# Performance work log

Hardware: AMD Instinct MI355X
Metric: run time of the kernel (lower is better)

## Reference

```python
import jax, jax.numpy as jnp
import numpy as np

E = 8        # num_experts
H = 2048     # hidden_size
I = 1408     # intermediate_size
K = 2        # top_k
B, S = 1, 2048


def setup_inputs() -> dict:
    key = jax.random.key(0)
    k1, k2, k3, k4, k5 = jax.random.split(key, 5)
    hidden_states = jax.random.normal(k1, (B, S, H), dtype=jnp.float32)
    top_k_index = jax.random.randint(k2, (B, S, K), 0, E, dtype=jnp.int32)
    top_k_weights = jax.random.uniform(k3, (B, S, K), dtype=jnp.float32)
    # scaled init so activations stay O(1)
    gate_up_proj = jax.random.normal(k4, (E, 2 * I, H), dtype=jnp.float32) / np.sqrt(H)
    down_proj = jax.random.normal(k5, (E, H, I), dtype=jnp.float32) / np.sqrt(I)
    return {
        "hidden_states": hidden_states,
        "top_k_index": top_k_index,
        "top_k_weights": top_k_weights,
        "gate_up_proj": gate_up_proj,
        "down_proj": down_proj,
    }


def reference(hidden_states, top_k_index, top_k_weights, gate_up_proj, down_proj):
    orig_shape = hidden_states.shape
    x = hidden_states.reshape(-1, H)            # [T, H]
    idx = top_k_index.reshape(-1, K)            # [T, K] int32
    w = top_k_weights.reshape(-1, K)            # [T, K]
    out = jnp.zeros_like(x)
    for e in range(E):
        # combine weight for tokens routed to expert e (0 if not routed)
        we = jnp.sum(w * (idx == e).astype(w.dtype), axis=-1)   # [T]
        gu = x @ gate_up_proj[e].T                              # [T, 2I]
        gate, up = gu[:, :I], gu[:, I:]
        h = jax.nn.silu(gate) * up                              # [T, I]
        y = h @ down_proj[e].T                                  # [T, H]
        out = out + we[:, None] * y
    return out.reshape(orig_shape)
```

## Files before the change

kernel.cpp:

```cpp
#include <hip/hip_runtime.h>
#include <hip/hip_bf16.h>

#define E_ 8
#define H_ 2048
#define I_ 1408
#define S_ 2048
#define NPAIR 4096
#define MAXMT 32

#define KT1 64
#define KT2 44

#define WGBLK 22528
#define WDBLK 11264
#define XBLK   2048

typedef short bf16x8 __attribute__((ext_vector_type(8)));
typedef ushort u16x8 __attribute__((ext_vector_type(8)));
typedef float f32x4  __attribute__((ext_vector_type(4)));

__device__ inline bf16x8 pack8(float4 a, float4 b) {
    bf16x8 r;
    const float v[8] = {a.x, a.y, a.z, a.w, b.x, b.y, b.z, b.w};
#pragma unroll
    for (int j = 0; j < 8; ++j) {
        __hip_bfloat16 t = __float2bfloat16(v[j]);
        r[j] = *reinterpret_cast<short*>(&t);
    }
    return r;
}

__device__ __forceinline__ void gload16(const ushort* g, ushort* l) {
    __builtin_amdgcn_global_load_lds(
        (const __attribute__((address_space(1))) void*)g,
        (__attribute__((address_space(3))) void*)l,
        16, 0, 0);
}

__global__ __launch_bounds__(256)
void convert_all(const float* __restrict__ wg, const float* __restrict__ wd,
                 const float* __restrict__ x, const int* __restrict__ tki,
                 ushort* __restrict__ wgb, ushort* __restrict__ wdb,
                 ushort* __restrict__ xb,
                 int* __restrict__ counts, int* __restrict__ bases,
                 int* __restrict__ tok, int* __restrict__ inv) {
    const int b = blockIdx.x;
    const int tid = threadIdx.x;
    if (b < WGBLK + WDBLK + XBLK) {
        const float* src;
        ushort* dst;
        size_t off;
        if (b < WGBLK)              { src = wg; dst = wgb; off = (size_t)b * 2048; }
        else if (b < WGBLK + WDBLK) { src = wd; dst = wdb; off = (size_t)(b - WGBLK) * 2048; }
        else                        { src = x;  dst = xb;  off = (size_t)(b - WGBLK - WDBLK) * 2048; }
        const size_t i = off + (size_t)tid * 8;
        const float4 a = *(const float4*)(src + i);
        const float4 c = *(const float4*)(src + i + 4);
        *(bf16x8*)(dst + i) = pack8(a, c);
        return;
    }
    __shared__ int cnt[E_];
    __shared__ int cur[E_];
    if (tid < E_) cnt[tid] = 0;
    __syncthreads();
    for (int p = tid; p < NPAIR; p += 256)
        atomicAdd(&cnt[tki[p]], 1);
    __syncthreads();
    if (tid == 0) {
        int bb = 0;
        for (int e = 0; e < E_; ++e) {
            counts[e] = cnt[e];
            bases[e]  = bb;
            cur[e]    = bb;
            bb += cnt[e];
        }
    }
    __syncthreads();
    for (int p = tid; p < NPAIR; p += 256) {
        const int e = tki[p];
        const int pos = atomicAdd(&cur[e], 1);
        tok[pos] = p >> 1;
        inv[p]   = pos;
    }
}

__global__ __launch_bounds__(256, 2)
void moe_gemm1(const ushort* __restrict__ xb,
               const ushort* __restrict__ wgb,
               const int* __restrict__ counts,
               const int* __restrict__ bases,
               const int* __restrict__ tok,
               ushort* __restrict__ hbuf) {
    const int e  = blockIdx.y & (E_ - 1);
    const int mt = blockIdx.y >> 3;
    const int count = counts[e];
    if (mt * 128 >= count) return;
    const int base = bases[e];
    const int nt = blockIdx.x;
    const int n0 = nt * 128;
    const ushort* wgbe = wgb + (size_t)e * (2 * I_) * H_;

    __shared__ alignas(16) ushort sm[24576];

    const int tid  = threadIdx.x;
    const int lane = tid & 63;
    const int wid  = tid >> 6;
    const int wm = wid & 1, wn = wid >> 1;
    const int lr = lane & 15, lq = lane >> 4;

    const f32x4 vzero = {0.f, 0.f, 0.f, 0.f};
    f32x4 accg[4][4], accu[4][4];
#pragma unroll
    for (int mi = 0; mi < 4; ++mi)
#pragma unroll
        for (int ni = 0; ni < 4; ++ni) { accg[mi][ni] = vzero; accu[mi][ni] = vzero; }

    const int srow = tid >> 2;
    const int sc8  = (tid & 3) * 8;
    const int ia0 = mt * 128 + srow, ia1 = ia0 + 64;
    const ushort* ap0 = xb + (size_t)(ia0 < count ? tok[base + ia0] : 0) * H_ + sc8;
    const ushort* ap1 = xb + (size_t)(ia1 < count ? tok[base + ia1] : 0) * H_ + sc8;
    const ushort* gp0 = wgbe + (size_t)(n0 + srow) * H_ + sc8;
    const ushort* gp1 = gp0 + (size_t)64 * H_;
    const ushort* up0 = wgbe + (size_t)(I_ + n0 + srow) * H_ + sc8;
    const ushort* up1 = up0 + (size_t)64 * H_;

    const int d0 = tid * 8, d1 = tid * 8 + 2048;

    {
        ushort* bA = sm; ushort* bG = sm + 4096; ushort* bU = sm + 8192;
        gload16(ap0, bA + d0); gload16(ap1, bA + d1);
        gload16(gp0, bG + d0); gload16(gp1, bG + d1);
        gload16(up0, bU + d0); gload16(up1, bU + d1);
    }

    for (int kt = 0; kt < KT1; ++kt) {
        ushort* curb = sm + (kt & 1) * 12288;
        if (kt + 1 < KT1) {
            ap0 += 32; ap1 += 32; gp0 += 32; gp1 += 32; up0 += 32; up1 += 32;
            ushort* nb = sm + ((kt + 1) & 1) * 12288;
            gload16(ap0, nb + d0);        gload16(ap1, nb + d1);
            gload16(gp0, nb + 4096 + d0); gload16(gp1, nb + 4096 + d1);
            gload16(up0, nb + 8192 + d0); gload16(up1, nb + 8192 + d1);
            asm volatile("s_waitcnt vmcnt(6)" ::: "memory");
        } else {
            asm volatile("s_waitcnt vmcnt(0)" ::: "memory");
        }
        __builtin_amdgcn_s_barrier();
        __builtin_amdgcn_sched_barrier(0);

        const ushort* As = curb;
        const ushort* Bg = curb + 4096;
        const ushort* Bu = curb + 8192;
        bf16x8 a[4], bg[4], bu[4];
#pragma unroll
        for (int mi = 0; mi < 4; ++mi)
            a[mi] = *(const bf16x8*)&As[(wm * 64 + mi * 16 + lr) * 32 + lq * 8];
#pragma unroll
        for (int ni = 0; ni < 4; ++ni) {
            bg[ni] = *(const bf16x8*)&Bg[(wn * 64 + ni * 16 + lr) * 32 + lq * 8];
            bu[ni] = *(const bf16x8*)&Bu[(wn * 64 + ni * 16 + lr) * 32 + lq * 8];
        }
#pragma unroll
        for (int mi = 0; mi < 4; ++mi)
#pragma unroll
            for (int ni = 0; ni < 4; ++ni) {
                accg[mi][ni] = __builtin_amdgcn_mfma_f32_16x16x32_bf16(a[mi], bg[ni], accg[mi][ni], 0, 0, 0);
                accu[mi][ni] = __builtin_amdgcn_mfma_f32_16x16x32_bf16(a[mi], bu[ni], accu[mi][ni], 0, 0, 0);
            }
        __builtin_amdgcn_sched_barrier(0);
        __builtin_amdgcn_s_barrier();
    }

    ushort* Ht = sm;
#pragma unroll
    for (int mi = 0; mi < 4; ++mi)
#pragma unroll
        for (int r = 0; r < 4; ++r) {
            const int row = wm * 64 + mi * 16 + lq * 4 + r;
#pragma unroll
            for (int ni = 0; ni < 4; ++ni) {
                const int col = wn * 64 + ni * 16 + lr;
                const float g = accg[mi][ni][r];
                const float u = accu[mi][ni][r];
                const float h = (g / (1.0f + __expf(-g))) * u;
                __hip_bfloat16 hb = __float2bfloat16(h);
                Ht[row * 136 + col] = *reinterpret_cast<ushort*>(&hb);
            }
        }
    __syncthreads();
#pragma unroll
    for (int p = 0; p < 8; ++p) {
        const int slot = p * 256 + tid;
        const int row = slot >> 4;
        const int cc  = (slot & 15) * 8;
        const int gi = mt * 128 + row;
        if (gi < count)
            *(uint4*)&hbuf[(size_t)(base + gi) * I_ + n0 + cc] = *(const uint4*)&Ht[row * 136 + cc];
    }
}

__global__ __launch_bounds__(256, 2)
void moe_gemm2(const ushort* __restrict__ hbuf,
               const ushort* __restrict__ wdb,
               const int* __restrict__ counts,
               const int* __restrict__ bases,
               ushort* __restrict__ ybuf) {
    const int e  = blockIdx.y & (E_ - 1);
    const int mt = blockIdx.y >> 3;
    const int count = counts[e];
    if (mt * 128 >= count) return;
    const int base = bases[e];
    const int nt = blockIdx.x;
    const int n0 = nt * 128;
    const ushort* wdbe = wdb + (size_t)e * H_ * I_;

    __shared__ alignas(16) ushort sm[17408];

    const int tid  = threadIdx.x;
    const int lane = tid & 63;
    const int wid  = tid >> 6;
    const int wm = wid & 1, wn = wid >> 1;
    const int lr = lane & 15, lq = lane >> 4;

    const f32x4 vzero = {0.f, 0.f, 0.f, 0.f};
    f32x4 acc[4][4];
#pragma unroll
    for (int mi = 0; mi < 4; ++mi)
#pragma unroll
        for (int ni = 0; ni < 4; ++ni) acc[mi][ni] = vzero;

    const int srow = tid >> 2;
    const int sc8  = (tid & 3) * 8;
    const int ia0 = mt * 128 + srow, ia1 = ia0 + 64;
    const ushort* ap0 = hbuf + (size_t)(base + (ia0 < count ? ia0 : 0)) * I_ + sc8;
    const ushort* ap1 = hbuf + (size_t)(base + (ia1 < count ? ia1 : 0)) * I_ + sc8;
    const ushort* bp0 = wdbe + (size_t)(n0 + srow) * I_ + sc8;
    const ushort* bp1 = bp0 + (size_t)64 * I_;

    const int d0 = tid * 8, d1 = tid * 8 + 2048;

    {
        ushort* bA = sm; ushort* bB = sm + 4096;
        gload16(ap0, bA + d0); gload16(ap1, bA + d1);
        gload16(bp0, bB + d0); gload16(bp1, bB + d1);
    }

    for (int kt = 0; kt < KT2; ++kt) {
        ushort* curb = sm + (kt & 1) * 8192;
        if (kt + 1 < KT2) {
            ap0 += 32; ap1 += 32; bp0 += 32; bp1 += 32;
            ushort* nb = sm + ((kt + 1) & 1) * 8192;
            gload16(ap0, nb + d0);        gload16(ap1, nb + d1);
            gload16(bp0, nb + 4096 + d0); gload16(bp1, nb + 4096 + d1);
            asm volatile("s_waitcnt vmcnt(4)" ::: "memory");
        } else {
            asm volatile("s_waitcnt vmcnt(0)" ::: "memory");
        }
        __builtin_amdgcn_s_barrier();
        __builtin_amdgcn_sched_barrier(0);

        const ushort* As = curb;
        const ushort* Bs = curb + 4096;
        bf16x8 a[4], b[4];
#pragma unroll
        for (int mi = 0; mi < 4; ++mi)
            a[mi] = *(const bf16x8*)&As[(wm * 64 + mi * 16 + lr) * 32 + lq * 8];
#pragma unroll
        for (int ni = 0; ni < 4; ++ni)
            b[ni] = *(const bf16x8*)&Bs[(wn * 64 + ni * 16 + lr) * 32 + lq * 8];
#pragma unroll
        for (int mi = 0; mi < 4; ++mi)
#pragma unroll
            for (int ni = 0; ni < 4; ++ni)
                acc[mi][ni] = __builtin_amdgcn_mfma_f32_16x16x32_bf16(a[mi], b[ni], acc[mi][ni], 0, 0, 0);
        __builtin_amdgcn_sched_barrier(0);
        __builtin_amdgcn_s_barrier();
    }

    ushort* Yt = sm;
#pragma unroll
    for (int mi = 0; mi < 4; ++mi)
#pragma unroll
        for (int r = 0; r < 4; ++r) {
            const int row = wm * 64 + mi * 16 + lq * 4 + r;
#pragma unroll
            for (int ni = 0; ni < 4; ++ni) {
                const int col = wn * 64 + ni * 16 + lr;
                __hip_bfloat16 yb = __float2bfloat16(acc[mi][ni][r]);
                Yt[row * 136 + col] = *reinterpret_cast<ushort*>(&yb);
            }
        }
    __syncthreads();
#pragma unroll
    for (int p = 0; p < 8; ++p) {
        const int slot = p * 256 + tid;
        const int row = slot >> 4;
        const int cc  = (slot & 15) * 8;
        const int gi = mt * 128 + row;
        if (gi < count)
            *(uint4*)&ybuf[(size_t)(base + gi) * H_ + n0 + cc] = *(const uint4*)&Yt[row * 136 + cc];
    }
}

__global__ void moe_combine(const ushort* __restrict__ ybuf,
                            const int* __restrict__ inv,
                            const float* __restrict__ tkw,
                            float* __restrict__ out) {
    const int t = blockIdx.x;
    const int c8 = threadIdx.x * 8;
    const int p0 = inv[2 * t], p1 = inv[2 * t + 1];
    const float w0 = tkw[2 * t], w1 = tkw[2 * t + 1];
    const u16x8 y0 = *(const u16x8*)(ybuf + (size_t)p0 * H_ + c8);
    const u16x8 y1 = *(const u16x8*)(ybuf + (size_t)p1 * H_ + c8);
    float o[8];
#pragma unroll
    for (int j = 0; j < 8; ++j) {
        const unsigned f0 = ((unsigned)y0[j]) << 16;
        const unsigned f1 = ((unsigned)y1[j]) << 16;
        o[j] = w0 * __uint_as_float(f0) + w1 * __uint_as_float(f1);
    }
    float* dst = out + (size_t)t * H_ + c8;
    *(float4*)dst       = make_float4(o[0], o[1], o[2], o[3]);
    *(float4*)(dst + 4) = make_float4(o[4], o[5], o[6], o[7]);
}

extern "C" void kernel_launch(void* const* d_in, const int* in_sizes, int n_in,
                              void* d_out, int out_size, void* d_ws, size_t ws_size,
                              hipStream_t stream) {
    const float* x   = (const float*)d_in[0];
    const int*   tki = (const int*)d_in[1];
    const float* tkw = (const float*)d_in[2];
    const float* wg  = (const float*)d_in[3];
    const float* wd  = (const float*)d_in[4];
    float* out = (float*)d_out;

    char* p = (char*)d_ws;
    int* counts = (int*)p;  p += 32;
    int* bases  = (int*)p;  p += 32;
    int* tok    = (int*)p;  p += NPAIR * sizeof(int);
    int* inv    = (int*)p;  p += NPAIR * sizeof(int);
    ushort* xb   = (ushort*)p; p += (size_t)S_ * H_ * 2;
    ushort* hbuf = (ushort*)p; p += (size_t)NPAIR * I_ * 2;
    ushort* ybuf = (ushort*)p; p += (size_t)NPAIR * H_ * 2;
    ushort* wgb  = (ushort*)p; p += (size_t)E_ * (2 * I_) * H_ * 2;
    ushort* wdb  = (ushort*)p; p += (size_t)E_ * H_ * I_ * 2;

    convert_all<<<dim3(WGBLK + WDBLK + XBLK + 1), 256, 0, stream>>>(
        wg, wd, x, tki, wgb, wdb, xb, counts, bases, tok, inv);
    moe_gemm1<<<dim3(I_ / 128, E_ * MAXMT), 256, 0, stream>>>(xb, wgb, counts, bases, tok, hbuf);
    moe_gemm2<<<dim3(H_ / 128, E_ * MAXMT), 256, 0, stream>>>(hbuf, wdb, counts, bases, ybuf);
    moe_combine<<<dim3(S_), 256, 0, stream>>>(ybuf, inv, tkw, out);
}
```

Measured before the change: 474.0 us.

## Use grid-stride conversion and loop over M tiles inside the MoE GEMM blocks

The fp32-to-bf16 conversion kernel now runs with a fixed 2048 blocks that grid-stride over the weight and activation chunks, instead of one block per chunk. Both grouped GEMM kernels launch only 4 M-slots per expert and loop over M tiles with stride 4. This replaces the old grid of 32 slots per expert, where most blocks exited early. The aim is to cut launch and empty-block overhead. The risk is that experts with more than 512 routed pairs now process their extra tile serially in the same block, which lengthens the tail of the GEMMs.

```diff
diff --git a/kernel.cpp b/kernel.cpp
--- a/kernel.cpp
+++ b/kernel.cpp
@@ -6,7 +6,6 @@
 #define I_ 1408
 #define S_ 2048
 #define NPAIR 4096
-#define MAXMT 32
 
 #define KT1 64
 #define KT2 44
@@ -14,6 +13,7 @@
 #define WGBLK 22528
 #define WDBLK 11264
 #define XBLK   2048
+#define CVT_BLOCKS 2048
 
 typedef short bf16x8 __attribute__((ext_vector_type(8)));
 typedef ushort u16x8 __attribute__((ext_vector_type(8)));
@@ -46,17 +46,26 @@
                  int* __restrict__ tok, int* __restrict__ inv) {
     const int b = blockIdx.x;
     const int tid = threadIdx.x;
-    if (b < WGBLK + WDBLK + XBLK) {
-        const float* src;
-        ushort* dst;
-        size_t off;
-        if (b < WGBLK)              { src = wg; dst = wgb; off = (size_t)b * 2048; }
-        else if (b < WGBLK + WDBLK) { src = wd; dst = wdb; off = (size_t)(b - WGBLK) * 2048; }
-        else                        { src = x;  dst = xb;  off = (size_t)(b - WGBLK - WDBLK) * 2048; }
-        const size_t i = off + (size_t)tid * 8;
-        const float4 a = *(const float4*)(src + i);
-        const float4 c = *(const float4*)(src + i + 4);
-        *(bf16x8*)(dst + i) = pack8(a, c);
+    if (b < CVT_BLOCKS) {
+        const int t8 = tid * 8;
+        for (int c = b; c < WGBLK; c += CVT_BLOCKS) {
+            const size_t i = (size_t)c * 2048 + t8;
+            const float4 a = *(const float4*)(wg + i);
+            const float4 d = *(const float4*)(wg + i + 4);
+            *(bf16x8*)(wgb + i) = pack8(a, d);
+        }
+        for (int c = b; c < WDBLK; c += CVT_BLOCKS) {
+            const size_t i = (size_t)c * 2048 + t8;
+            const float4 a = *(const float4*)(wd + i);
+            const float4 d = *(const float4*)(wd + i + 4);
+            *(bf16x8*)(wdb + i) = pack8(a, d);
+        }
+        for (int c = b; c < XBLK; c += CVT_BLOCKS) {
+            const size_t i = (size_t)c * 2048 + t8;
+            const float4 a = *(const float4*)(x + i);
+            const float4 d = *(const float4*)(x + i + 4);
+            *(bf16x8*)(xb + i) = pack8(a, d);
+        }
         return;
     }
     __shared__ int cnt[E_];
@@ -92,9 +101,8 @@
                const int* __restrict__ tok,
                ushort* __restrict__ hbuf) {
     const int e  = blockIdx.y & (E_ - 1);
-    const int mt = blockIdx.y >> 3;
+    const int m0 = blockIdx.y >> 3;
     const int count = counts[e];
-    if (mt * 128 >= count) return;
     const int base = bases[e];
     const int nt = blockIdx.x;
     const int n0 = nt * 128;
@@ -108,95 +116,98 @@
     const int wm = wid & 1, wn = wid >> 1;
     const int lr = lane & 15, lq = lane >> 4;
 
-    const f32x4 vzero = {0.f, 0.f, 0.f, 0.f};
-    f32x4 accg[4][4], accu[4][4];
-#pragma unroll
-    for (int mi = 0; mi < 4; ++mi)
-#pragma unroll
-        for (int ni = 0; ni < 4; ++ni) { accg[mi][ni] = vzero; accu[mi][ni] = vzero; }
-
     const int srow = tid >> 2;
     const int sc8  = (tid & 3) * 8;
-    const int ia0 = mt * 128 + srow, ia1 = ia0 + 64;
-    const ushort* ap0 = xb + (size_t)(ia0 < count ? tok[base + ia0] : 0) * H_ + sc8;
-    const ushort* ap1 = xb + (size_t)(ia1 < count ? tok[base + ia1] : 0) * H_ + sc8;
-    const ushort* gp0 = wgbe + (size_t)(n0 + srow) * H_ + sc8;
-    const ushort* gp1 = gp0 + (size_t)64 * H_;
-    const ushort* up0 = wgbe + (size_t)(I_ + n0 + srow) * H_ + sc8;
-    const ushort* up1 = up0 + (size_t)64 * H_;
-
     const int d0 = tid * 8, d1 = tid * 8 + 2048;
-
-    {
-        ushort* bA = sm; ushort* bG = sm + 4096; ushort* bU = sm + 8192;
-        gload16(ap0, bA + d0); gload16(ap1, bA + d1);
-        gload16(gp0, bG + d0); gload16(gp1, bG + d1);
-        gload16(up0, bU + d0); gload16(up1, bU + d1);
-    }
-
-    for (int kt = 0; kt < KT1; ++kt) {
-        ushort* curb = sm + (kt & 1) * 12288;
-        if (kt + 1 < KT1) {
-            ap0 += 32; ap1 += 32; gp0 += 32; gp1 += 32; up0 += 32; up1 += 32;
-            ushort* nb = sm + ((kt + 1) & 1) * 12288;
-            gload16(ap0, nb + d0);        gload16(ap1, nb + d1);
-            gload16(gp0, nb + 4096 + d0); gload16(gp1, nb + 4096 + d1);
-            gload16(up0, nb + 8192 + d0); gload16(up1, nb + 8192 + d1);
-            asm volatile("s_waitcnt vmcnt(6)" ::: "memory");
-        } else {
-            asm volatile("s_waitcnt vmcnt(0)" ::: "memory");
-        }
-        __builtin_amdgcn_s_barrier();
-        __builtin_amdgcn_sched_barrier(0);
-
-        const ushort* As = curb;
-        const ushort* Bg = curb + 4096;
-        const ushort* Bu = curb + 8192;
-        bf16x8 a[4], bg[4], bu[4];
+    const f32x4 vzero = {0.f, 0.f, 0.f, 0.f};
+
+    for (int mt = m0; mt * 128 < count; mt += 4) {
+        f32x4 accg[4][4], accu[4][4];
 #pragma unroll
         for (int mi = 0; mi < 4; ++mi)
-            a[mi] = *(const bf16x8*)&As[(wm * 64 + mi * 16 + lr) * 32 + lq * 8];
-#pragma unroll
-        for (int ni = 0; ni < 4; ++ni) {
-            bg[ni] = *(const bf16x8*)&Bg[(wn * 64 + ni * 16 + lr) * 32 + lq * 8];
-            bu[ni] = *(const bf16x8*)&Bu[(wn * 64 + ni * 16 + lr) * 32 + lq * 8];
-        }
+#pragma unroll
+            for (int ni = 0; ni < 4; ++ni) { accg[mi][ni] = vzero; accu[mi][ni] = vzero; }
+
+        const int ia0 = mt * 128 + srow, ia1 = ia0 + 64;
+        const ushort* ap0 = xb + (size_t)(ia0 < count ? tok[base + ia0] : 0) * H_ + sc8;
+        const ushort* ap1 = xb + (size_t)(ia1 < count ? tok[base + ia1] : 0) * H_ + sc8;
+        const ushort* gp0 = wgbe + (size_t)(n0 + srow) * H_ + sc8;
+        const ushort* gp1 = gp0 + (size_t)64 * H_;
+        const ushort* up0 = wgbe + (size_t)(I_ + n0 + srow) * H_ + sc8;
+        const ushort* up1 = up0 + (size_t)64 * H_;
+
+        {
+            ushort* bA = sm; ushort* bG = sm + 4096; ushort* bU = sm + 8192;
+            gload16(ap0, bA + d0); gload16(ap1, bA + d1);
+            gload16(gp0, bG + d0); gload16(gp1, bG + d1);
+            gload16(up0, bU + d0); gload16(up1, bU + d1);
+        }
+
+        for (int kt = 0; kt < KT1; ++kt) {
+            ushort* curb = sm + (kt & 1) * 12288;
+            if (kt + 1 < KT1) {
+                ap0 += 32; ap1 += 32; gp0 += 32; gp1 += 32; up0 += 32; up1 += 32;
+                ushort* nb = sm + ((kt + 1) & 1) * 12288;
+                gload16(ap0, nb + d0);        gload16(ap1, nb + d1);
+                gload16(gp0, nb + 4096 + d0); gload16(gp1, nb + 4096 + d1);
+                gload16(up0, nb + 8192 + d0); gload16(up1, nb + 8192 + d1);
+                asm volatile("s_waitcnt vmcnt(6)" ::: "memory");
+            } else {
+                asm volatile("s_waitcnt vmcnt(0)" ::: "memory");
+            }
+            __builtin_amdgcn_s_barrier();
+            __builtin_amdgcn_sched_barrier(0);
+
+            const ushort* As = curb;
+            const ushort* Bg = curb + 4096;
+            const ushort* Bu = curb + 8192;
+            bf16x8 a[4], bg[4], bu[4];
+#pragma unroll
+            for (int mi = 0; mi < 4; ++mi)
+                a[mi] = *(const bf16x8*)&As[(wm * 64 + mi * 16 + lr) * 32 + lq * 8];
+#pragma unroll
+            for (int ni = 0; ni < 4; ++ni) {
+                bg[ni] = *(const bf16x8*)&Bg[(wn * 64 + ni * 16 + lr) * 32 + lq * 8];
+                bu[ni] = *(const bf16x8*)&Bu[(wn * 64 + ni * 16 + lr) * 32 + lq * 8];
+            }
+#pragma unroll
+            for (int mi = 0; mi < 4; ++mi)
+#pragma unroll
+                for (int ni = 0; ni < 4; ++ni) {
+                    accg[mi][ni] = __builtin_amdgcn_mfma_f32_16x16x32_bf16(a[mi], bg[ni], accg[mi][ni], 0, 0, 0);
+                    accu[mi][ni] = __builtin_amdgcn_mfma_f32_16x16x32_bf16(a[mi], bu[ni], accu[mi][ni], 0, 0, 0);
+                }
+            __builtin_amdgcn_sched_barrier(0);
+            __builtin_amdgcn_s_barrier();
+        }
+
+        ushort* Ht = sm;
 #pragma unroll
         for (int mi = 0; mi < 4; ++mi)
 #pragma unroll
-            for (int ni = 0; ni < 4; ++ni) {
-                accg[mi][ni] = __builtin_amdgcn_mfma_f32_16x16x32_bf16(a[mi], bg[ni], accg[mi][ni], 0, 0, 0);
-                accu[mi][ni] = __builtin_amdgcn_mfma_f32_16x16x32_bf16(a[mi], bu[ni], accu[mi][ni], 0, 0, 0);
-            }
-        __builtin_amdgcn_sched_barrier(0);
-        __builtin_amdgcn_s_barrier();
-    }
-
-    ushort* Ht = sm;
-#pragma unroll
-    for (int mi = 0; mi < 4; ++mi)
-#pragma unroll
-        for (int r = 0; r < 4; ++r) {
-            const int row = wm * 64 + mi * 16 + lq * 4 + r;
-#pragma unroll
-            for (int ni = 0; ni < 4; ++ni) {
-                const int col = wn * 64 + ni * 16 + lr;
-                const float g = accg[mi][ni][r];
-                const float u = accu[mi][ni][r];
-                const float h = (g / (1.0f + __expf(-g))) * u;
-                __hip_bfloat16 hb = __float2bfloat16(h);
-                Ht[row * 136 + col] = *reinterpret_cast<ushort*>(&hb);
-            }
-        }
-    __syncthreads();
-#pragma unroll
-    for (int p = 0; p < 8; ++p) {
-        const int slot = p * 256 + tid;
-        const int row = slot >> 4;
-        const int cc  = (slot & 15) * 8;
-        const int gi = mt * 128 + row;
-        if (gi < count)
-            *(uint4*)&hbuf[(size_t)(base + gi) * I_ + n0 + cc] = *(const uint4*)&Ht[row * 136 + cc];
+            for (int r = 0; r < 4; ++r) {
+                const int row = wm * 64 + mi * 16 + lq * 4 + r;
+#pragma unroll
+                for (int ni = 0; ni < 4; ++ni) {
+                    const int col = wn * 64 + ni * 16 + lr;
+                    const float g = accg[mi][ni][r];
+                    const float u = accu[mi][ni][r];
+                    const float h = (g / (1.0f + __expf(-g))) * u;
+                    __hip_bfloat16 hb = __float2bfloat16(h);
+                    Ht[row * 136 + col] = *reinterpret_cast<ushort*>(&hb);
+                }
+            }
+        __syncthreads();
+#pragma unroll
+        for (int p = 0; p < 8; ++p) {
+            const int slot = p * 256 + tid;
+            const int row = slot >> 4;
+            const int cc  = (slot & 15) * 8;
+            const int gi = mt * 128 + row;
+            if (gi < count)
+                *(uint4*)&hbuf[(size_t)(base + gi) * I_ + n0 + cc] = *(const uint4*)&Ht[row * 136 + cc];
+        }
+        __syncthreads();
     }
 }
 
@@ -207,9 +218,8 @@
                const int* __restrict__ bases,
                ushort* __restrict__ ybuf) {
     const int e  = blockIdx.y & (E_ - 1);
-    const int mt = blockIdx.y >> 3;
+    const int m0 = blockIdx.y >> 3;
     const int count = counts[e];
-    if (mt * 128 >= count) return;
     const int base = bases[e];
     const int nt = blockIdx.x;
     const int n0 = nt * 128;
@@ -223,83 +233,86 @@
     const int wm = wid & 1, wn = wid >> 1;
     const int lr = lane & 15, lq = lane >> 4;
 
-    const f32x4 vzero = {0.f, 0.f, 0.f, 0.f};
-    f32x4 acc[4][4];
-#pragma unroll
-    for (int mi = 0; mi < 4; ++mi)
-#pragma unroll
-        for (int ni = 0; ni < 4; ++ni) acc[mi][ni] = vzero;
-
     const int srow = tid >> 2;
     const int sc8  = (tid & 3) * 8;
-    const int ia0 = mt * 128 + srow, ia1 = ia0 + 64;
-    const ushort* ap0 = hbuf + (size_t)(base + (ia0 < count ? ia0 : 0)) * I_ + sc8;
-    const ushort* ap1 = hbuf + (size_t)(base + (ia1 < count ? ia1 : 0)) * I_ + sc8;
-    const ushort* bp0 = wdbe + (size_t)(n0 + srow) * I_ + sc8;
-    const ushort* bp1 = bp0 + (size_t)64 * I_;
-
     const int d0 = tid * 8, d1 = tid * 8 + 2048;
-
-    {
-        ushort* bA = sm; ushort* bB = sm + 4096;
-        gload16(ap0, bA + d0); gload16(ap1, bA + d1);
-        gload16(bp0, bB + d0); gload16(bp1, bB + d1);
-    }
-
-    for (int kt = 0; kt < KT2; ++kt) {
-        ushort* curb = sm + (kt & 1) * 8192;
-        if (kt + 1 < KT2) {
-            ap0 += 32; ap1 += 32; bp0 += 32; bp1 += 32;
-            ushort* nb = sm + ((kt + 1) & 1) * 8192;
-            gload16(ap0, nb + d0);        gload16(ap1, nb + d1);
-            gload16(bp0, nb + 4096 + d0); gload16(bp1, nb + 4096 + d1);
-            asm volatile("s_waitcnt vmcnt(4)" ::: "memory");
-        } else {
-            asm volatile("s_waitcnt vmcnt(0)" ::: "memory");
-        }
-        __builtin_amdgcn_s_barrier();
-        __builtin_amdgcn_sched_barrier(0);
-
-        const ushort* As = curb;
-        const ushort* Bs = curb + 4096;
-        bf16x8 a[4], b[4];
+    const f32x4 vzero = {0.f, 0.f, 0.f, 0.f};
+
+    for (int mt = m0; mt * 128 < count; mt += 4) {
+        f32x4 acc[4][4];
 #pragma unroll
         for (int mi = 0; mi < 4; ++mi)
-            a[mi] = *(const bf16x8*)&As[(wm * 64 + mi * 16 + lr) * 32 + lq * 8];
-#pragma unroll
-        for (int ni = 0; ni < 4; ++ni)
-            b[ni] = *(const bf16x8*)&Bs[(wn * 64 + ni * 16 + lr) * 32 + lq * 8];
+#pragma unroll
+            for (int ni = 0; ni < 4; ++ni) acc[mi][ni] = vzero;
+
+        const int ia0 = mt * 128 + srow, ia1 = ia0 + 64;
+        const ushort* ap0 = hbuf + (size_t)(base + (ia0 < count ? ia0 : 0)) * I_ + sc8;
+        const ushort* ap1 = hbuf + (size_t)(base + (ia1 < count ? ia1 : 0)) * I_ + sc8;
+        const ushort* bp0 = wdbe + (size_t)(n0 + srow) * I_ + sc8;
+        const ushort* bp1 = bp0 + (size_t)64 * I_;
+
+        {
+            ushort* bA = sm; ushort* bB = sm + 4096;
+            gload16(ap0, bA + d0); gload16(ap1, bA + d1);
+            gload16(bp0, bB + d0); gload16(bp1, bB + d1);
+        }
+
+        for (int kt = 0; kt < KT2; ++kt) {
+            ushort* curb = sm + (kt & 1) * 8192;
+            if (kt + 1 < KT2) {
+                ap0 += 32; ap1 += 32; bp0 += 32; bp1 += 32;
+                ushort* nb = sm + ((kt + 1) & 1) * 8192;
+                gload16(ap0, nb + d0);        gload16(ap1, nb + d1);
+                gload16(bp0, nb + 4096 + d0); gload16(bp1, nb + 4096 + d1);
+                asm volatile("s_waitcnt vmcnt(4)" ::: "memory");
+            } else {
+                asm volatile("s_waitcnt vmcnt(0)" ::: "memory");
+            }
+            __builtin_amdgcn_s_barrier();
+            __builtin_amdgcn_sched_barrier(0);
+
+            const ushort* As = curb;
+            const ushort* Bs = curb + 4096;
+            bf16x8 a[4], b[4];
+#pragma unroll
+            for (int mi = 0; mi < 4; ++mi)
+                a[mi] = *(const bf16x8*)&As[(wm * 64 + mi * 16 + lr) * 32 + lq * 8];
+#pragma unroll
+            for (int ni = 0; ni < 4; ++ni)
+                b[ni] = *(const bf16x8*)&Bs[(wn * 64 + ni * 16 + lr) * 32 + lq * 8];
+#pragma unroll
+            for (int mi = 0; mi < 4; ++mi)
+#pragma unroll
+                for (int ni = 0; ni < 4; ++ni)
+                    acc[mi][ni] = __builtin_amdgcn_mfma_f32_16x16x32_bf16(a[mi], b[ni], acc[mi][ni], 0, 0, 0);
+            __builtin_amdgcn_sched_barrier(0);
+            __builtin_amdgcn_s_barrier();
+        }
+
+        ushort* Yt = sm;
 #pragma unroll
         for (int mi = 0; mi < 4; ++mi)
 #pragma unroll
-            for (int ni = 0; ni < 4; ++ni)
-                acc[mi][ni] = __builtin_amdgcn_mfma_f32_16x16x32_bf16(a[mi], b[ni], acc[mi][ni], 0, 0, 0);
-        __builtin_amdgcn_sched_barrier(0);
-        __builtin_amdgcn_s_barrier();
-    }
-
-    ushort* Yt = sm;
-#pragma unroll
-    for (int mi = 0; mi < 4; ++mi)
-#pragma unroll
-        for (int r = 0; r < 4; ++r) {
-            const int row = wm * 64 + mi * 16 + lq * 4 + r;
-#pragma unroll
-            for (int ni = 0; ni < 4; ++ni) {
-                const int col = wn * 64 + ni * 16 + lr;
-                __hip_bfloat16 yb = __float2bfloat16(acc[mi][ni][r]);
-                Yt[row * 136 + col] = *reinterpret_cast<ushort*>(&yb);
-            }
-        }
-    __syncthreads();
-#pragma unroll
-    for (int p = 0; p < 8; ++p) {
-        const int slot = p * 256 + tid;
-        const int row = slot >> 4;
-        const int cc  = (slot & 15) * 8;
-        const int gi = mt * 128 + row;
-        if (gi < count)
-            *(uint4*)&ybuf[(size_t)(base + gi) * H_ + n0 + cc] = *(const uint4*)&Yt[row * 136 + cc];
+            for (int r = 0; r < 4; ++r) {
+                const int row = wm * 64 + mi * 16 + lq * 4 + r;
+#pragma unroll
+                for (int ni = 0; ni < 4; ++ni) {
+                    const int col = wn * 64 + ni * 16 + lr;
+                    __hip_bfloat16 yb = __float2bfloat16(acc[mi][ni][r]);
+                    Yt[row * 136 + col] = *reinterpret_cast<ushort*>(&yb);
+                }
+            }
+        __syncthreads();
+#pragma unroll
+        for (int p = 0; p < 8; ++p) {
+            const int slot = p * 256 + tid;
+            const int row = slot >> 4;
+            const int cc  = (slot & 15) * 8;
+            const int gi = mt * 128 + row;
+            if (gi < count)
+                *(uint4*)&ybuf[(size_t)(base + gi) * H_ + n0 + cc] = *(const uint4*)&Yt[row * 136 + cc];
+        }
+        __syncthreads();
     }
 }
 
@@ -346,9 +359,9 @@
     ushort* wgb  = (ushort*)p; p += (size_t)E_ * (2 * I_) * H_ * 2;
     ushort* wdb  = (ushort*)p; p += (size_t)E_ * H_ * I_ * 2;
 
-    convert_all<<<dim3(WGBLK + WDBLK + XBLK + 1), 256, 0, stream>>>(
+    convert_all<<<dim3(CVT_BLOCKS + 1), 256, 0, stream>>>(
         wg, wd, x, tki, wgb, wdb, xb, counts, bases, tok, inv);
-    moe_gemm1<<<dim3(I_ / 128, E_ * MAXMT), 256, 0, stream>>>(xb, wgb, counts, bases, tok, hbuf);
-    moe_gemm2<<<dim3(H_ / 128, E_ * MAXMT), 256, 0, stream>>>(hbuf, wdb, counts, bases, ybuf);
+    moe_gemm1<<<dim3(I_ / 128, E_ * 4), 256, 0, stream>>>(xb, wgb, counts, bases, tok, hbuf);
+    moe_gemm2<<<dim3(H_ / 128, E_ * 4), 256, 0, stream>>>(hbuf, wdb, counts, bases, ybuf);
     moe_combine<<<dim3(S_), 256, 0, stream>>>(ybuf, inv, tkw, out);
 }
```

Measured after the change: 508.2 us. 7.2% more time.

## Fuse down-proj weight conversion into gemm1 and use persistent M-tile loops

Applied to the files above, without the earlier changes.

The fp32-to-bf16 conversion of the down-projection weights moves out of the standalone convert kernel and into the start of every gemm1 block, with each of the 704 blocks converting 16 chunks. The aim is to overlap that conversion traffic with gemm1 compute and shrink the convert pass. Both GEMMs also drop the fixed 32-M-tile grid (mostly early-exit blocks) for 8 blocks per expert that loop over M tiles with stride 8, which cuts idle block launches. In exchange, long-tailed experts are serialized within fewer blocks, and the conversion adds memory traffic at the head of gemm1.

```diff
diff --git a/kernel.cpp b/kernel.cpp
--- a/kernel.cpp
+++ b/kernel.cpp
@@ -6,14 +6,14 @@
 #define I_ 1408
 #define S_ 2048
 #define NPAIR 4096
-#define MAXMT 32
 
 #define KT1 64
 #define KT2 44
 
 #define WGBLK 22528
+#define XBLK   2048
 #define WDBLK 11264
-#define XBLK   2048
+#define WD_PER_BLK 16
 
 typedef short bf16x8 __attribute__((ext_vector_type(8)));
 typedef ushort u16x8 __attribute__((ext_vector_type(8)));
@@ -38,21 +38,19 @@
 }
 
 __global__ __launch_bounds__(256)
-void convert_all(const float* __restrict__ wg, const float* __restrict__ wd,
-                 const float* __restrict__ x, const int* __restrict__ tki,
-                 ushort* __restrict__ wgb, ushort* __restrict__ wdb,
-                 ushort* __restrict__ xb,
+void convert_all(const float* __restrict__ wg, const float* __restrict__ x,
+                 const int* __restrict__ tki,
+                 ushort* __restrict__ wgb, ushort* __restrict__ xb,
                  int* __restrict__ counts, int* __restrict__ bases,
                  int* __restrict__ tok, int* __restrict__ inv) {
     const int b = blockIdx.x;
     const int tid = threadIdx.x;
-    if (b < WGBLK + WDBLK + XBLK) {
+    if (b < WGBLK + XBLK) {
         const float* src;
         ushort* dst;
         size_t off;
-        if (b < WGBLK)              { src = wg; dst = wgb; off = (size_t)b * 2048; }
-        else if (b < WGBLK + WDBLK) { src = wd; dst = wdb; off = (size_t)(b - WGBLK) * 2048; }
-        else                        { src = x;  dst = xb;  off = (size_t)(b - WGBLK - WDBLK) * 2048; }
+        if (b < WGBLK) { src = wg; dst = wgb; off = (size_t)b * 2048; }
+        else           { src = x;  dst = xb;  off = (size_t)(b - WGBLK) * 2048; }
         const size_t i = off + (size_t)tid * 8;
         const float4 a = *(const float4*)(src + i);
         const float4 c = *(const float4*)(src + i + 4);
@@ -87,14 +85,29 @@
 __global__ __launch_bounds__(256, 2)
 void moe_gemm1(const ushort* __restrict__ xb,
                const ushort* __restrict__ wgb,
+               const float* __restrict__ wd,
+               ushort* __restrict__ wdb,
                const int* __restrict__ counts,
                const int* __restrict__ bases,
                const int* __restrict__ tok,
                ushort* __restrict__ hbuf) {
+    const int tid  = threadIdx.x;
+
+    {
+        const int bid = blockIdx.y * gridDim.x + blockIdx.x;
+        const size_t t8 = (size_t)tid * 8;
+#pragma unroll
+        for (int j = 0; j < WD_PER_BLK; ++j) {
+            const size_t i = ((size_t)(bid * WD_PER_BLK + j)) * 2048 + t8;
+            const float4 a = *(const float4*)(wd + i);
+            const float4 c = *(const float4*)(wd + i + 4);
+            *(bf16x8*)(wdb + i) = pack8(a, c);
+        }
+    }
+
     const int e  = blockIdx.y & (E_ - 1);
-    const int mt = blockIdx.y >> 3;
+    const int m0 = blockIdx.y >> 3;
     const int count = counts[e];
-    if (mt * 128 >= count) return;
     const int base = bases[e];
     const int nt = blockIdx.x;
     const int n0 = nt * 128;
@@ -102,101 +115,103 @@
 
     __shared__ alignas(16) ushort sm[24576];
 
-    const int tid  = threadIdx.x;
     const int lane = tid & 63;
     const int wid  = tid >> 6;
     const int wm = wid & 1, wn = wid >> 1;
     const int lr = lane & 15, lq = lane >> 4;
 
-    const f32x4 vzero = {0.f, 0.f, 0.f, 0.f};
-    f32x4 accg[4][4], accu[4][4];
-#pragma unroll
-    for (int mi = 0; mi < 4; ++mi)
-#pragma unroll
-        for (int ni = 0; ni < 4; ++ni) { accg[mi][ni] = vzero; accu[mi][ni] = vzero; }
-
     const int srow = tid >> 2;
     const int sc8  = (tid & 3) * 8;
-    const int ia0 = mt * 128 + srow, ia1 = ia0 + 64;
-    const ushort* ap0 = xb + (size_t)(ia0 < count ? tok[base + ia0] : 0) * H_ + sc8;
-    const ushort* ap1 = xb + (size_t)(ia1 < count ? tok[base + ia1] : 0) * H_ + sc8;
-    const ushort* gp0 = wgbe + (size_t)(n0 + srow) * H_ + sc8;
-    const ushort* gp1 = gp0 + (size_t)64 * H_;
-    const ushort* up0 = wgbe + (size_t)(I_ + n0 + srow) * H_ + sc8;
-    const ushort* up1 = up0 + (size_t)64 * H_;
-
     const int d0 = tid * 8, d1 = tid * 8 + 2048;
-
-    {
-        ushort* bA = sm; ushort* bG = sm + 4096; ushort* bU = sm + 8192;
-        gload16(ap0, bA + d0); gload16(ap1, bA + d1);
-        gload16(gp0, bG + d0); gload16(gp1, bG + d1);
-        gload16(up0, bU + d0); gload16(up1, bU + d1);
-    }
-
-    for (int kt = 0; kt < KT1; ++kt) {
-        ushort* curb = sm + (kt & 1) * 12288;
-        if (kt + 1 < KT1) {
-            ap0 += 32; ap1 += 32; gp0 += 32; gp1 += 32; up0 += 32; up1 += 32;
-            ushort* nb = sm + ((kt + 1) & 1) * 12288;
-            gload16(ap0, nb + d0);        gload16(ap1, nb + d1);
-            gload16(gp0, nb + 4096 + d0); gload16(gp1, nb + 4096 + d1);
-            gload16(up0, nb + 8192 + d0); gload16(up1, nb + 8192 + d1);
-            asm volatile("s_waitcnt vmcnt(6)" ::: "memory");
-        } else {
-            asm volatile("s_waitcnt vmcnt(0)" ::: "memory");
-        }
-        __builtin_amdgcn_s_barrier();
-        __builtin_amdgcn_sched_barrier(0);
-
-        const ushort* As = curb;
-        const ushort* Bg = curb + 4096;
-        const ushort* Bu = curb + 8192;
-        bf16x8 a[4], bg[4], bu[4];
+    const f32x4 vzero = {0.f, 0.f, 0.f, 0.f};
+
+    for (int mt = m0; mt * 128 < count; mt += 8) {
+        f32x4 accg[4][4], accu[4][4];
 #pragma unroll
         for (int mi = 0; mi < 4; ++mi)
-            a[mi] = *(const bf16x8*)&As[(wm * 64 + mi * 16 + lr) * 32 + lq * 8];
-#pragma unroll
-        for (int ni = 0; ni < 4; ++ni) {
-            bg[ni] = *(const bf16x8*)&Bg[(wn * 64 + ni * 16 + lr) * 32 + lq * 8];
-            bu[ni] = *(const bf16x8*)&Bu[(wn * 64 + ni * 16 + lr) * 32 + lq * 8];
-        }
+#pragma unroll
+            for (int ni = 0; ni < 4; ++ni) { accg[mi][ni] = vzero; accu[mi][ni] = vzero; }
+
+        const int ia0 = mt * 128 + srow, ia1 = ia0 + 64;
+        const ushort* ap0 = xb + (size_t)(ia0 < count ? tok[base + ia0] : 0) * H_ + sc8;
+        const ushort* ap1 = xb + (size_t)(ia1 < count ? tok[base + ia1] : 0) * H_ + sc8;
+        const ushort* gp0 = wgbe + (size_t)(n0 + srow) * H_ + sc8;
+        const ushort* gp1 = gp0 + (size_t)64 * H_;
+        const ushort* up0 = wgbe + (size_t)(I_ + n0 + srow) * H_ + sc8;
+        const ushort* up1 = up0 + (size_t)64 * H_;
+
+        {
+            ushort* bA = sm; ushort* bG = sm + 4096; ushort* bU = sm + 8192;
+            gload16(ap0, bA + d0); gload16(ap1, bA + d1);
+            gload16(gp0, bG + d0); gload16(gp1, bG + d1);
+            gload16(up0, bU + d0); gload16(up1, bU + d1);
+        }
+
+        for (int kt = 0; kt < KT1; ++kt) {
+            ushort* curb = sm + (kt & 1) * 12288;
+            if (kt + 1 < KT1) {
+                ap0 += 32; ap1 += 32; gp0 += 32; gp1 += 32; up0 += 32; up1 += 32;
+                ushort* nb = sm + ((kt + 1) & 1) * 12288;
+                gload16(ap0, nb + d0);        gload16(ap1, nb + d1);
+                gload16(gp0, nb + 4096 + d0); gload16(gp1, nb + 4096 + d1);
+                gload16(up0, nb + 8192 + d0); gload16(up1, nb + 8192 + d1);
+                asm volatile("s_waitcnt vmcnt(6)" ::: "memory");
+            } else {
+                asm volatile("s_waitcnt vmcnt(0)" ::: "memory");
+            }
+            __builtin_amdgcn_s_barrier();
+            __builtin_amdgcn_sched_barrier(0);
+
+            const ushort* As = curb;
+            const ushort* Bg = curb + 4096;
+            const ushort* Bu = curb + 8192;
+            bf16x8 a[4], bg[4], bu[4];
+#pragma unroll
+            for (int mi = 0; mi < 4; ++mi)
+                a[mi] = *(const bf16x8*)&As[(wm * 64 + mi * 16 + lr) * 32 + lq * 8];
+#pragma unroll
+            for (int ni = 0; ni < 4; ++ni) {
+                bg[ni] = *(const bf16x8*)&Bg[(wn * 64 + ni * 16 + lr) * 32 + lq * 8];
+                bu[ni] = *(const bf16x8*)&Bu[(wn * 64 + ni * 16 + lr) * 32 + lq * 8];
+            }
+#pragma unroll
+            for (int mi = 0; mi < 4; ++mi)
+#pragma unroll
+                for (int ni = 0; ni < 4; ++ni) {
+                    accg[mi][ni] = __builtin_amdgcn_mfma_f32_16x16x32_bf16(a[mi], bg[ni], accg[mi][ni], 0, 0, 0);
+                    accu[mi][ni] = __builtin_amdgcn_mfma_f32_16x16x32_bf16(a[mi], bu[ni], accu[mi][ni], 0, 0, 0);
+                }
+            __builtin_amdgcn_sched_barrier(0);
+            __builtin_amdgcn_s_barrier();
+        }
+
+        ushort* Ht = sm;
 #pragma unroll
         for (int mi = 0; mi < 4; ++mi)
 #pragma unroll
-            for (int ni = 0; ni < 4; ++ni) {
-                accg[mi][ni] = __builtin_amdgcn_mfma_f32_16x16x32_bf16(a[mi], bg[ni], accg[mi][ni], 0, 0, 0);
-                accu[mi][ni] = __builtin_amdgcn_mfma_f32_16x16x32_bf16(a[mi], bu[ni], accu[mi][ni], 0, 0, 0);
-            }
-        __builtin_amdgcn_sched_barrier(0);
-        __builtin_amdgcn_s_barrier();
-    }
-
-    ushort* Ht = sm;
-#pragma unroll
-    for (int mi = 0; mi < 4; ++mi)
-#pragma unroll
-        for (int r = 0; r < 4; ++r) {
-            const int row = wm * 64 + mi * 16 + lq * 4 + r;
-#pragma unroll
-            for (int ni = 0; ni < 4; ++ni) {
-                const int col = wn * 64 + ni * 16 + lr;
-                const float g = accg[mi][ni][r];
-                const float u = accu[mi][ni][r];
-                const float h = (g / (1.0f + __expf(-g))) * u;
-                __hip_bfloat16 hb = __float2bfloat16(h);
-                Ht[row * 136 + col] = *reinterpret_cast<ushort*>(&hb);
-            }
-        }
-    __syncthreads();
-#pragma unroll
-    for (int p = 0; p < 8; ++p) {
-        const int slot = p * 256 + tid;
-        const int row = slot >> 4;
-        const int cc  = (slot & 15) * 8;
-        const int gi = mt * 128 + row;
-        if (gi < count)
-            *(uint4*)&hbuf[(size_t)(base + gi) * I_ + n0 + cc] = *(const uint4*)&Ht[row * 136 + cc];
+            for (int r = 0; r < 4; ++r) {
+                const int row = wm * 64 + mi * 16 + lq * 4 + r;
+#pragma unroll
+                for (int ni = 0; ni < 4; ++ni) {
+                    const int col = wn * 64 + ni * 16 + lr;
+                    const float g = accg[mi][ni][r];
+                    const float u = accu[mi][ni][r];
+                    const float h = (g / (1.0f + __expf(-g))) * u;
+                    __hip_bfloat16 hb = __float2bfloat16(h);
+                    Ht[row * 136 + col] = *reinterpret_cast<ushort*>(&hb);
+                }
+            }
+        __syncthreads();
+#pragma unroll
+        for (int p = 0; p < 8; ++p) {
+            const int slot = p * 256 + tid;
+            const int row = slot >> 4;
+            const int cc  = (slot & 15) * 8;
+            const int gi = mt * 128 + row;
+            if (gi < count)
+                *(uint4*)&hbuf[(size_t)(base + gi) * I_ + n0 + cc] = *(const uint4*)&Ht[row * 136 + cc];
+        }
+        __syncthreads();
     }
 }
 
@@ -207,9 +222,8 @@
                const int* __restrict__ bases,
                ushort* __restrict__ ybuf) {
     const int e  = blockIdx.y & (E_ - 1);
-    const int mt = blockIdx.y >> 3;
+    const int m0 = blockIdx.y >> 3;
     const int count = counts[e];
-    if (mt * 128 >= count) return;
     const int base = bases[e];
     const int nt = blockIdx.x;
     const int n0 = nt * 128;
@@ -223,83 +237,86 @@
     const int wm = wid & 1, wn = wid >> 1;
     const int lr = lane & 15, lq = lane >> 4;
 
-    const f32x4 vzero = {0.f, 0.f, 0.f, 0.f};
-    f32x4 acc[4][4];
-#pragma unroll
-    for (int mi = 0; mi < 4; ++mi)
-#pragma unroll
-        for (int ni = 0; ni < 4; ++ni) acc[mi][ni] = vzero;
-
     const int srow = tid >> 2;
     const int sc8  = (tid & 3) * 8;
-    const int ia0 = mt * 128 + srow, ia1 = ia0 + 64;
-    const ushort* ap0 = hbuf + (size_t)(base + (ia0 < count ? ia0 : 0)) * I_ + sc8;
-    const ushort* ap1 = hbuf + (size_t)(base + (ia1 < count ? ia1 : 0)) * I_ + sc8;
-    const ushort* bp0 = wdbe + (size_t)(n0 + srow) * I_ + sc8;
-    const ushort* bp1 = bp0 + (size_t)64 * I_;
-
     const int d0 = tid * 8, d1 = tid * 8 + 2048;
-
-    {
-        ushort* bA = sm; ushort* bB = sm + 4096;
-        gload16(ap0, bA + d0); gload16(ap1, bA + d1);
-        gload16(bp0, bB + d0); gload16(bp1, bB + d1);
-    }
-
-    for (int kt = 0; kt < KT2; ++kt) {
-        ushort* curb = sm + (kt & 1) * 8192;
-        if (kt + 1 < KT2) {
-            ap0 += 32; ap1 += 32; bp0 += 32; bp1 += 32;
-            ushort* nb = sm + ((kt + 1) & 1) * 8192;
-            gload16(ap0, nb + d0);        gload16(ap1, nb + d1);
-            gload16(bp0, nb + 4096 + d0); gload16(bp1, nb + 4096 + d1);
-            asm volatile("s_waitcnt vmcnt(4)" ::: "memory");
-        } else {
-            asm volatile("s_waitcnt vmcnt(0)" ::: "memory");
-        }
-        __builtin_amdgcn_s_barrier();
-        __builtin_amdgcn_sched_barrier(0);
-
-        const ushort* As = curb;
-        const ushort* Bs = curb + 4096;
-        bf16x8 a[4], b[4];
+    const f32x4 vzero = {0.f, 0.f, 0.f, 0.f};
+
+    for (int mt = m0; mt * 128 < count; mt += 8) {
+        f32x4 acc[4][4];
 #pragma unroll
         for (int mi = 0; mi < 4; ++mi)
-            a[mi] = *(const bf16x8*)&As[(wm * 64 + mi * 16 + lr) * 32 + lq * 8];
-#pragma unroll
-        for (int ni = 0; ni < 4; ++ni)
-            b[ni] = *(const bf16x8*)&Bs[(wn * 64 + ni * 16 + lr) * 32 + lq * 8];
+#pragma unroll
+            for (int ni = 0; ni < 4; ++ni) acc[mi][ni] = vzero;
+
+        const int ia0 = mt * 128 + srow, ia1 = ia0 + 64;
+        const ushort* ap0 = hbuf + (size_t)(base + (ia0 < count ? ia0 : 0)) * I_ + sc8;
+        const ushort* ap1 = hbuf + (size_t)(base + (ia1 < count ? ia1 : 0)) * I_ + sc8;
+        const ushort* bp0 = wdbe + (size_t)(n0 + srow) * I_ + sc8;
+        const ushort* bp1 = bp0 + (size_t)64 * I_;
+
+        {
+            ushort* bA = sm; ushort* bB = sm + 4096;
+            gload16(ap0, bA + d0); gload16(ap1, bA + d1);
+            gload16(bp0, bB + d0); gload16(bp1, bB + d1);
+        }
+
+        for (int kt = 0; kt < KT2; ++kt) {
+            ushort* curb = sm + (kt & 1) * 8192;
+            if (kt + 1 < KT2) {
+                ap0 += 32; ap1 += 32; bp0 += 32; bp1 += 32;
+                ushort* nb = sm + ((kt + 1) & 1) * 8192;
+                gload16(ap0, nb + d0);        gload16(ap1, nb + d1);
+                gload16(bp0, nb + 4096 + d0); gload16(bp1, nb + 4096 + d1);
+                asm volatile("s_waitcnt vmcnt(4)" ::: "memory");
+            } else {
+                asm volatile("s_waitcnt vmcnt(0)" ::: "memory");
+            }
+            __builtin_amdgcn_s_barrier();
+            __builtin_amdgcn_sched_barrier(0);
+
+            const ushort* As = curb;
+            const ushort* Bs = curb + 4096;
+            bf16x8 a[4], b[4];
+#pragma unroll
+            for (int mi = 0; mi < 4; ++mi)
+                a[mi] = *(const bf16x8*)&As[(wm * 64 + mi * 16 + lr) * 32 + lq * 8];
+#pragma unroll
+            for (int ni = 0; ni < 4; ++ni)
+                b[ni] = *(const bf16x8*)&Bs[(wn * 64 + ni * 16 + lr) * 32 + lq * 8];
+#pragma unroll
+            for (int mi = 0; mi < 4; ++mi)
+#pragma unroll
+                for (int ni = 0; ni < 4; ++ni)
+                    acc[mi][ni] = __builtin_amdgcn_mfma_f32_16x16x32_bf16(a[mi], b[ni], acc[mi][ni], 0, 0, 0);
+            __builtin_amdgcn_sched_barrier(0);
+            __builtin_amdgcn_s_barrier();
+        }
+
+        ushort* Yt = sm;
 #pragma unroll
         for (int mi = 0; mi < 4; ++mi)
 #pragma unroll
-            for (int ni = 0; ni < 4; ++ni)
-                acc[mi][ni] = __builtin_amdgcn_mfma_f32_16x16x32_bf16(a[mi], b[ni], acc[mi][ni], 0, 0, 0);
-        __builtin_amdgcn_sched_barrier(0);
-        __builtin_amdgcn_s_barrier();
-    }
-
-    ushort* Yt = sm;
-#pragma unroll
-    for (int mi = 0; mi < 4; ++mi)
-#pragma unroll
-        for (int r = 0; r < 4; ++r) {
-            const int row = wm * 64 + mi * 16 + lq * 4 + r;
-#pragma unroll
-            for (int ni = 0; ni < 4; ++ni) {
-                const int col = wn * 64 + ni * 16 + lr;
-                __hip_bfloat16 yb = __float2bfloat16(acc[mi][ni][r]);
-                Yt[row * 136 + col] = *reinterpret_cast<ushort*>(&yb);
-            }
-        }
-    __syncthreads();
-#pragma unroll
-    for (int p = 0; p < 8; ++p) {
-        const int slot = p * 256 + tid;
-        const int row = slot >> 4;
-        const int cc  = (slot & 15) * 8;
-        const int gi = mt * 128 + row;
-        if (gi < count)
-            *(uint4*)&ybuf[(size_t)(base + gi) * H_ + n0 + cc] = *(const uint4*)&Yt[row * 136 + cc];
+            for (int r = 0; r < 4; ++r) {
+                const int row = wm * 64 + mi * 16 + lq * 4 + r;
+#pragma unroll
+                for (int ni = 0; ni < 4; ++ni) {
+                    const int col = wn * 64 + ni * 16 + lr;
+                    __hip_bfloat16 yb = __float2bfloat16(acc[mi][ni][r]);
+                    Yt[row * 136 + col] = *reinterpret_cast<ushort*>(&yb);
+                }
+            }
+        __syncthreads();
+#pragma unroll
+        for (int p = 0; p < 8; ++p) {
+            const int slot = p * 256 + tid;
+            const int row = slot >> 4;
+            const int cc  = (slot & 15) * 8;
+            const int gi = mt * 128 + row;
+            if (gi < count)
+                *(uint4*)&ybuf[(size_t)(base + gi) * H_ + n0 + cc] = *(const uint4*)&Yt[row * 136 + cc];
+        }
+        __syncthreads();
     }
 }
 
@@ -346,9 +363,10 @@
     ushort* wgb  = (ushort*)p; p += (size_t)E_ * (2 * I_) * H_ * 2;
     ushort* wdb  = (ushort*)p; p += (size_t)E_ * H_ * I_ * 2;
 
-    convert_all<<<dim3(WGBLK + WDBLK + XBLK + 1), 256, 0, stream>>>(
-        wg, wd, x, tki, wgb, wdb, xb, counts, bases, tok, inv);
-    moe_gemm1<<<dim3(I_ / 128, E_ * MAXMT), 256, 0, stream>>>(xb, wgb, counts, bases, tok, hbuf);
-    moe_gemm2<<<dim3(H_ / 128, E_ * MAXMT), 256, 0, stream>>>(hbuf, wdb, counts, bases, ybuf);
+    convert_all<<<dim3(WGBLK + XBLK + 1), 256, 0, stream>>>(
+        wg, x, tki, wgb, xb, counts, bases, tok, inv);
+    moe_gemm1<<<dim3(I_ / 128, E_ * 8), 256, 0, stream>>>(
+        xb, wgb, wd, wdb, counts, bases, tok, hbuf);
+    moe_gemm2<<<dim3(H_ / 128, E_ * 8), 256, 0, stream>>>(hbuf, wdb, counts, bases, ybuf);
     moe_combine<<<dim3(S_), 256, 0, stream>>>(ybuf, inv, tkw, out);
 }
```

Result: no change. 466.3 us (-1.6%).
